# Kernel tuning notes

Hardware: AMD Instinct MI355X
Metric: run time of the kernel (lower is better)

Reference implementation:

```python
import jax, jax.numpy as jnp
import numpy as np

B = 16
S_IN, S_DIM, Z_DIM, PE_DIM = 21, 256, 64, 64
REGIONS = ["cdr3", "pep", "mhc", "hv", "hj", "lv", "lj"]
LENS = {"cdr3": 24, "pep": 16, "mhc": 48, "hv": 104, "hj": 16, "lv": 104, "lj": 14}
L_TOTAL = 1 + sum(LENS.values())  # 327 = collapse token + all regions (full masks)
N_COND = 6


def _pos_enc(L):
    # sinusoidal PE matching one_d_positional_encoding: sin for even i, cos for odd i,
    # both with divisor 10000**(i/dim)
    pos = jnp.arange(L, dtype=jnp.float32)
    i = jnp.arange(PE_DIM)
    ang = pos[:, None] / (10000.0 ** (i.astype(jnp.float32) / PE_DIM))
    return jnp.where(i % 2 == 0, jnp.sin(ang), jnp.cos(ang))  # [L, 64]


def _pair_id():
    # region label per position: 0=psi, 1=cdr3, 2..7 = conditioning regions in order
    reg = np.concatenate([[0]] + [[k + 1] * LENS[r] for k, r in enumerate(REGIONS)])
    reg = jnp.asarray(reg, dtype=jnp.int32)
    ri, rj = reg[:, None], reg[None, :]
    i = jnp.arange(L_TOTAL, dtype=jnp.int32)[:, None]
    j = jnp.arange(L_TOTAL, dtype=jnp.int32)[None, :]
    p = jnp.zeros((L_TOTAL, L_TOTAL), dtype=jnp.int32)
    p = jnp.where((i == 0) | (j == 0), 1, p)                    # lvl1: psi <-> all
    p = jnp.where((i == 0) & (j == 0), 0, p)                    # lvl0: psi self
    cb = (ri == 1) & (rj == 1)
    p = jnp.where(cb & (jnp.abs(i - j) == 1), 2, p)             # lvl2: cdr3 sequential
    p = jnp.where(cb & (i != j) & (jnp.abs(i - j) != 1), 3, p)  # lvl3: cdr3 internal
    p = jnp.where(((ri == 1) & (rj >= 2)) | ((ri >= 2) & (rj == 1)), 4, p)  # lvl4
    p = jnp.where((ri >= 2) & (ri == rj), 5 + (ri - 2), p)      # lvl5..10: cond internal
    a = jnp.minimum(ri, rj) - 2
    b = jnp.maximum(ri, rj) - 2
    cross = a * (2 * N_COND - a - 1) // 2 + (b - a - 1)         # upper-tri pair index
    p = jnp.where((ri >= 2) & (rj >= 2) & (ri != rj), 11 + cross, p)  # lvl11..25
    return jnp.minimum(p, 31)


def _region_emb(seq, w2, seq_W, seq_b, pos_W, pos_b):
    # seq: [B, Lr, 21] -> [B, Lr, 256]
    se = jnp.einsum('bld,ed->ble', seq, seq_W) + seq_b
    pe = _pos_enc(seq.shape[1]) @ pos_W.T + pos_b  # [Lr, 256]
    return w2[0] * se + w2[1] * pe


def setup_inputs() -> dict:
    key = jax.random.key(0)
    ks = jax.random.split(key, 16)
    inp = {}
    for n, (name, r) in enumerate(zip(
            ['cdr3_xt', 'pep_seq', 'mhc_seq', 'hv_seq', 'hj_seq', 'lv_seq', 'lj_seq'], REGIONS)):
        inp[name] = jax.random.normal(ks[n], (B, LENS[r], S_IN), dtype=jnp.float32)
    inp['seq_W'] = jax.random.normal(ks[7], (S_DIM, S_IN), dtype=jnp.float32) * 0.1
    inp['seq_b'] = jnp.zeros((S_DIM,), dtype=jnp.float32)
    inp['pos_W'] = jax.random.normal(ks[8], (S_DIM, PE_DIM), dtype=jnp.float32) * 0.1
    inp['pos_b'] = jnp.zeros((S_DIM,), dtype=jnp.float32)
    inp['pair1_W'] = jax.random.normal(ks[9], (Z_DIM // 2, 8), dtype=jnp.float32) * 0.3
    inp['pair1_b'] = jnp.zeros((Z_DIM // 2,), dtype=jnp.float32)
    inp['pair2_W'] = jax.random.normal(ks[10], (Z_DIM // 2, 4), dtype=jnp.float32) * 0.3
    inp['pair2_b'] = jnp.zeros((Z_DIM // 2,), dtype=jnp.float32)
    inp['collapse_token'] = jax.random.normal(ks[11], (1, S_DIM), dtype=jnp.float32) * 0.1
    inp['collapse_weight'] = jnp.ones((1,), dtype=jnp.float32)
    inp['region_w'] = jax.random.uniform(ks[12], (7, 2), dtype=jnp.float32) + 0.5
    for name, r in zip(['cdr3_mask', 'pep_mask', 'mhc_mask', 'hv_mask', 'hj_mask', 'lv_mask', 'lj_mask'], REGIONS):
        inp[name] = jnp.ones((B, LENS[r]), dtype=jnp.int32)
    return inp


def reference(cdr3_xt, pep_seq, mhc_seq, hv_seq, hj_seq, lv_seq, lj_seq,
              seq_W, seq_b, pos_W, pos_b, pair1_W, pair1_b, pair2_W, pair2_b,
              collapse_token, collapse_weight, region_w,
              cdr3_mask, pep_mask, mhc_mask, hv_mask, hj_mask, lv_mask, lj_mask):
    # masks are all-ones -> every region is full-length (static shapes); they are
    # only used in torch to derive lengths, so they are closed-over constants here.
    seqs = [cdr3_xt, pep_seq, mhc_seq, hv_seq, hj_seq, lv_seq, lj_seq]
    parts = [jnp.broadcast_to(collapse_weight * collapse_token, (B, 1, S_DIM))]
    for k, seq in enumerate(seqs):
        parts.append(_region_emb(seq, region_w[k], seq_W, seq_b, pos_W, pos_b))
    s = jnp.concatenate(parts, axis=1)  # [B, 327, 256]
    p = _pair_id()                      # [327, 327] int32, identical across batch
    # one_hot(k, n) @ W.T + b  ==  (W.T + b)[k]  -> pure gather from tiny tables
    t1 = pair1_W.T + pair1_b            # [8, 32]
    t2 = pair2_W.T + pair2_b            # [4, 32]
    z = jnp.concatenate([t1[p // 4], t2[p % 4]], axis=-1)        # [327, 327, 64]
    z = jnp.broadcast_to(z[None], (B, L_TOTAL, L_TOTAL, Z_DIM))  # per-sample z list -> stacked
    return s, z
```

## Files before the change

kernel.cpp:

```cpp
#include <hip/hip_runtime.h>
#include <math.h>

#define NB 16
#define LTOT 327
#define SDIM 256
#define ZD 64

__device__ __constant__ int d_starts[7] = {1, 25, 41, 89, 193, 209, 313};
__device__ __constant__ int d_lens[7]   = {24, 16, 48, 104, 16, 104, 14};

__device__ __forceinline__ int regid(int x) {
    return (x >= 1) + (x >= 25) + (x >= 41) + (x >= 89) + (x >= 193) + (x >= 209) + (x >= 313);
}

__device__ __forceinline__ int pair_id(int i, int j, int ri, int rj) {
    if ((i == 0) && (j == 0)) return 0;
    if ((i == 0) || (j == 0)) return 1;
    if ((ri == 1) && (rj == 1)) {
        int d = i > j ? i - j : j - i;
        if (d == 1) return 2;
        if (d != 0) return 3;
        return 0;
    }
    if ((ri == 1) || (rj == 1)) return 4;
    if (ri == rj) return 5 + ri - 2;
    int a = (ri < rj ? ri : rj) - 2;
    int c = (ri < rj ? rj : ri) - 2;
    return 11 + a * (11 - a) / 2 + (c - a - 1);
}

__global__ __launch_bounds__(256) void s_kernel(
    const float* __restrict__ s0, const float* __restrict__ s1,
    const float* __restrict__ s2, const float* __restrict__ s3,
    const float* __restrict__ s4, const float* __restrict__ s5,
    const float* __restrict__ s6,
    const float* __restrict__ seqW, const float* __restrict__ seqb,
    const float* __restrict__ posW, const float* __restrict__ posb,
    const float* __restrict__ ctok, const float* __restrict__ cw,
    const float* __restrict__ rw,
    float* __restrict__ out)
{
    int blk = blockIdx.x;
    int l = blk % LTOT;
    int b = blk / LTOT;
    int e = threadIdx.x;

    if (l == 0) {
        out[(size_t)blk * SDIM + e] = cw[0] * ctok[e];
        return;
    }

    __shared__ float sh_seq[21];
    __shared__ float sh_pe[64];

    int k = (l >= 25) + (l >= 41) + (l >= 89) + (l >= 193) + (l >= 209) + (l >= 313);
    int pl = l - d_starts[k];

    const float* sp;
    switch (k) {
        case 0: sp = s0; break; case 1: sp = s1; break; case 2: sp = s2; break;
        case 3: sp = s3; break; case 4: sp = s4; break; case 5: sp = s5; break;
        default: sp = s6;
    }
    if (e < 21) sh_seq[e] = sp[((size_t)b * d_lens[k] + pl) * 21 + e];
    if (e < 64) {
        float scale = exp2f(-(float)e * (13.287712379549449f / 64.0f));
        float ang = (float)pl * scale;
        sh_pe[e] = (e & 1) ? cosf(ang) : sinf(ang);
    }
    __syncthreads();

    float se = seqb[e];
    const float* wrow = seqW + e * 21;
    #pragma unroll
    for (int d = 0; d < 21; d++) se = fmaf(sh_seq[d], wrow[d], se);

    float pe = posb[e];
    const float* pwrow = posW + e * 64;
    #pragma unroll 8
    for (int i2 = 0; i2 < 64; i2++) pe = fmaf(sh_pe[i2], pwrow[i2], pe);

    float w0 = rw[2 * k], w1 = rw[2 * k + 1];
    out[(size_t)blk * SDIM + e] = w0 * se + w1 * pe;
}

#define TSTRIDE 68

__global__ __launch_bounds__(256) void z_kernel(
    const float* __restrict__ p1W, const float* __restrict__ p1b,
    const float* __restrict__ p2W, const float* __restrict__ p2b,
    float* __restrict__ outz)
{
    __shared__ __align__(16) float table[32 * TSTRIDE];
    __shared__ int pr[LTOT];

    int t = threadIdx.x;

    for (int idx = t; idx < 32 * 64; idx += 256) {
        int p = idx >> 6, c = idx & 63;
        float v;
        if (c < 32) v = p1W[c * 8 + (p >> 2)] + p1b[c];
        else        v = p2W[(c - 32) * 4 + (p & 3)] + p2b[c - 32];
        table[p * TSTRIDE + c] = v;
    }

    int blk = blockIdx.x;
    int i = blk % LTOT;
    int ri = regid(i);
    for (int j = t; j < LTOT; j += 256) pr[j] = pair_id(i, j, ri, regid(j));
    __syncthreads();

    float4* dst = (float4*)(outz + (size_t)blk * (LTOT * ZD));
    const int NF4 = LTOT * (ZD / 4);
    for (int idx = t; idx < NF4; idx += 256) {
        int j = idx >> 4, c4 = idx & 15;
        const float4* src = (const float4*)(table + pr[j] * TSTRIDE + c4 * 4);
        dst[idx] = *src;
    }
}

extern "C" void kernel_launch(void* const* d_in, const int* in_sizes, int n_in,
                              void* d_out, int out_size, void* d_ws, size_t ws_size,
                              hipStream_t stream) {
    const float* seq0 = (const float*)d_in[0];
    const float* seq1 = (const float*)d_in[1];
    const float* seq2 = (const float*)d_in[2];
    const float* seq3 = (const float*)d_in[3];
    const float* seq4 = (const float*)d_in[4];
    const float* seq5 = (const float*)d_in[5];
    const float* seq6 = (const float*)d_in[6];
    const float* seqW = (const float*)d_in[7];
    const float* seqb = (const float*)d_in[8];
    const float* posW = (const float*)d_in[9];
    const float* posb = (const float*)d_in[10];
    const float* p1W  = (const float*)d_in[11];
    const float* p1b  = (const float*)d_in[12];
    const float* p2W  = (const float*)d_in[13];
    const float* p2b  = (const float*)d_in[14];
    const float* ctok = (const float*)d_in[15];
    const float* cw   = (const float*)d_in[16];
    const float* rw   = (const float*)d_in[17];

    float* out = (float*)d_out;
    float* outz = out + (size_t)NB * LTOT * SDIM;

    s_kernel<<<NB * LTOT, 256, 0, stream>>>(seq0, seq1, seq2, seq3, seq4, seq5, seq6,
                                            seqW, seqb, posW, posb, ctok, cw, rw, out);
    z_kernel<<<NB * LTOT, 256, 0, stream>>>(p1W, p1b, p2W, p2b, outz);
}
```

Before: 543.1 us.

## Hoist positional encoding out of batch loop and write z by region segments

Positional-encoding projections are computed once per position into workspace by a new kernel, since they do not depend on the batch. The s kernel then only does the 21-wide sequence projection and adds the precomputed term. The z kernel drops the per-column pair-id shared array and writes each region segment with one table value, handling the cdr3-cdr3 diagonal band specially. Kernel launch order changes and one launch is added; the fallback is used only if the workspace is too small.

```diff
diff --git a/kernel.cpp b/kernel.cpp
--- a/kernel.cpp
+++ b/kernel.cpp
@@ -8,6 +8,9 @@
 
 __device__ __constant__ int d_starts[7] = {1, 25, 41, 89, 193, 209, 313};
 __device__ __constant__ int d_lens[7]   = {24, 16, 48, 104, 16, 104, 14};
+
+__device__ __constant__ int seg_s[8] = {0, 1, 25, 41, 89, 193, 209, 313};
+__device__ __constant__ int seg_e[8] = {1, 25, 41, 89, 193, 209, 313, 327};
 
 __device__ __forceinline__ int regid(int x) {
     return (x >= 1) + (x >= 25) + (x >= 41) + (x >= 89) + (x >= 193) + (x >= 209) + (x >= 313);
@@ -27,6 +30,69 @@
     int a = (ri < rj ? ri : rj) - 2;
     int c = (ri < rj ? rj : ri) - 2;
     return 11 + a * (11 - a) / 2 + (c - a - 1);
+}
+
+__global__ __launch_bounds__(256) void pe_kernel(
+    const float* __restrict__ posW, const float* __restrict__ posb,
+    const float* __restrict__ rw, float* __restrict__ pe_full)
+{
+    int l = blockIdx.x;
+    int e = threadIdx.x;
+    __shared__ float sh_pe[64];
+
+    int k = (l >= 25) + (l >= 41) + (l >= 89) + (l >= 193) + (l >= 209) + (l >= 313);
+    int pl = (l == 0) ? 0 : (l - d_starts[k]);
+    if (e < 64) {
+        float scale = exp2f(-(float)e * (13.287712379549449f / 64.0f));
+        float ang = (float)pl * scale;
+        sh_pe[e] = (e & 1) ? cosf(ang) : sinf(ang);
+    }
+    __syncthreads();
+
+    float pe = posb[e];
+    const float* pwrow = posW + e * 64;
+    #pragma unroll 8
+    for (int i2 = 0; i2 < 64; i2++) pe = fmaf(sh_pe[i2], pwrow[i2], pe);
+    pe_full[(size_t)l * SDIM + e] = rw[2 * k + 1] * pe;
+}
+
+__global__ __launch_bounds__(256) void s_kernel2(
+    const float* __restrict__ s0, const float* __restrict__ s1,
+    const float* __restrict__ s2, const float* __restrict__ s3,
+    const float* __restrict__ s4, const float* __restrict__ s5,
+    const float* __restrict__ s6,
+    const float* __restrict__ seqW, const float* __restrict__ seqb,
+    const float* __restrict__ ctok, const float* __restrict__ cw,
+    const float* __restrict__ rw, const float* __restrict__ pe_full,
+    float* __restrict__ out)
+{
+    int blk = blockIdx.x;
+    int l = blk % LTOT;
+    int b = blk / LTOT;
+    int e = threadIdx.x;
+
+    if (l == 0) {
+        out[(size_t)blk * SDIM + e] = cw[0] * ctok[e];
+        return;
+    }
+    __shared__ float sh_seq[21];
+    int k = (l >= 25) + (l >= 41) + (l >= 89) + (l >= 193) + (l >= 209) + (l >= 313);
+    int pl = l - d_starts[k];
+    const float* sp;
+    switch (k) {
+        case 0: sp = s0; break; case 1: sp = s1; break; case 2: sp = s2; break;
+        case 3: sp = s3; break; case 4: sp = s4; break; case 5: sp = s5; break;
+        default: sp = s6;
+    }
+    if (e < 21) sh_seq[e] = sp[((size_t)b * d_lens[k] + pl) * 21 + e];
+    __syncthreads();
+
+    float se = seqb[e];
+    const float* wrow = seqW + e * 21;
+    #pragma unroll
+    for (int d = 0; d < 21; d++) se = fmaf(sh_seq[d], wrow[d], se);
+
+    out[(size_t)blk * SDIM + e] = rw[2 * k] * se + pe_full[(size_t)l * SDIM + e];
 }
 
 __global__ __launch_bounds__(256) void s_kernel(
@@ -44,18 +110,11 @@
     int l = blk % LTOT;
     int b = blk / LTOT;
     int e = threadIdx.x;
-
-    if (l == 0) {
-        out[(size_t)blk * SDIM + e] = cw[0] * ctok[e];
-        return;
-    }
-
+    if (l == 0) { out[(size_t)blk * SDIM + e] = cw[0] * ctok[e]; return; }
     __shared__ float sh_seq[21];
     __shared__ float sh_pe[64];
-
     int k = (l >= 25) + (l >= 41) + (l >= 89) + (l >= 193) + (l >= 209) + (l >= 313);
     int pl = l - d_starts[k];
-
     const float* sp;
     switch (k) {
         case 0: sp = s0; break; case 1: sp = s1; break; case 2: sp = s2; break;
@@ -69,19 +128,15 @@
         sh_pe[e] = (e & 1) ? cosf(ang) : sinf(ang);
     }
     __syncthreads();
-
     float se = seqb[e];
     const float* wrow = seqW + e * 21;
     #pragma unroll
     for (int d = 0; d < 21; d++) se = fmaf(sh_seq[d], wrow[d], se);
-
     float pe = posb[e];
     const float* pwrow = posW + e * 64;
     #pragma unroll 8
     for (int i2 = 0; i2 < 64; i2++) pe = fmaf(sh_pe[i2], pwrow[i2], pe);
-
-    float w0 = rw[2 * k], w1 = rw[2 * k + 1];
-    out[(size_t)blk * SDIM + e] = w0 * se + w1 * pe;
+    out[(size_t)blk * SDIM + e] = rw[2 * k] * se + rw[2 * k + 1] * pe;
 }
 
 #define TSTRIDE 68
@@ -92,8 +147,6 @@
     float* __restrict__ outz)
 {
     __shared__ __align__(16) float table[32 * TSTRIDE];
-    __shared__ int pr[LTOT];
-
     int t = threadIdx.x;
 
     for (int idx = t; idx < 32 * 64; idx += 256) {
@@ -103,19 +156,35 @@
         else        v = p2W[(c - 32) * 4 + (p & 3)] + p2b[c - 32];
         table[p * TSTRIDE + c] = v;
     }
+    __syncthreads();
 
     int blk = blockIdx.x;
     int i = blk % LTOT;
     int ri = regid(i);
-    for (int j = t; j < LTOT; j += 256) pr[j] = pair_id(i, j, ri, regid(j));
-    __syncthreads();
+    int c4 = t & 15;
+    int jo = t >> 4;
 
     float4* dst = (float4*)(outz + (size_t)blk * (LTOT * ZD));
-    const int NF4 = LTOT * (ZD / 4);
-    for (int idx = t; idx < NF4; idx += 256) {
-        int j = idx >> 4, c4 = idx & 15;
-        const float4* src = (const float4*)(table + pr[j] * TSTRIDE + c4 * 4);
-        dst[idx] = *src;
+
+    #pragma unroll
+    for (int s = 0; s < 8; s++) {
+        int js = seg_s[s], je = seg_e[s];
+        if (ri == 1 && s == 1) {
+            float4 v0 = *(const float4*)(table + 0 * TSTRIDE + c4 * 4);
+            float4 v2 = *(const float4*)(table + 2 * TSTRIDE + c4 * 4);
+            float4 v3 = *(const float4*)(table + 3 * TSTRIDE + c4 * 4);
+            for (int j = js + jo; j < je; j += 16) {
+                int d = i > j ? i - j : j - i;
+                float4 v = (d == 0) ? v0 : ((d == 1) ? v2 : v3);
+                dst[j * 16 + c4] = v;
+            }
+        } else {
+            int p = pair_id(i, js, ri, regid(js));
+            float4 v = *(const float4*)(table + p * TSTRIDE + c4 * 4);
+            for (int j = js + jo; j < je; j += 16) {
+                dst[j * 16 + c4] = v;
+            }
+        }
     }
 }
 
@@ -144,7 +213,15 @@
     float* out = (float*)d_out;
     float* outz = out + (size_t)NB * LTOT * SDIM;
 
-    s_kernel<<<NB * LTOT, 256, 0, stream>>>(seq0, seq1, seq2, seq3, seq4, seq5, seq6,
-                                            seqW, seqb, posW, posb, ctok, cw, rw, out);
     z_kernel<<<NB * LTOT, 256, 0, stream>>>(p1W, p1b, p2W, p2b, outz);
-}
+
+    if (ws_size >= (size_t)LTOT * SDIM * sizeof(float)) {
+        float* pe_full = (float*)d_ws;
+        pe_kernel<<<LTOT, 256, 0, stream>>>(posW, posb, rw, pe_full);
+        s_kernel2<<<NB * LTOT, 256, 0, stream>>>(seq0, seq1, seq2, seq3, seq4, seq5, seq6,
+                                                 seqW, seqb, ctok, cw, rw, pe_full, out);
+    } else {
+        s_kernel<<<NB * LTOT, 256, 0, stream>>>(seq0, seq1, seq2, seq3, seq4, seq5, seq6,
+                                                seqW, seqb, posW, posb, ctok, cw, rw, out);
+    }
+}
```

Measured after the change: 509.8 us (median of 2 runs). 6.1% less time.

## Fuse s and z kernels, specialize z writes per region with nontemporal stores

Applied to the files above, without the earlier changes.

Merges the s-embedding and z-pair kernels into one launch, with the z blocks placed first and the s blocks after them. The z path no longer builds a per-row pair-id array in shared memory. It loops over the 8 static region segments, loads one table vector per segment (the cdr3-cdr3 block picks per element), and writes it with nontemporal stores. This removes a launch and most of the per-element shared-memory gathers on a write-bound output of about 27M floats, at the cost of a more complex control flow.

```diff
diff --git a/kernel.cpp b/kernel.cpp
--- a/kernel.cpp
+++ b/kernel.cpp
@@ -5,9 +5,9 @@
 #define LTOT 327
 #define SDIM 256
 #define ZD 64
+#define ZROWS (NB * LTOT)
 
-__device__ __constant__ int d_starts[7] = {1, 25, 41, 89, 193, 209, 313};
-__device__ __constant__ int d_lens[7]   = {24, 16, 48, 104, 16, 104, 14};
+typedef float vf4 __attribute__((ext_vector_type(4)));
 
 __device__ __forceinline__ int regid(int x) {
     return (x >= 1) + (x >= 25) + (x >= 41) + (x >= 89) + (x >= 193) + (x >= 209) + (x >= 313);
@@ -29,93 +29,104 @@
     return 11 + a * (11 - a) / 2 + (c - a - 1);
 }
 
-__global__ __launch_bounds__(256) void s_kernel(
+__global__ __launch_bounds__(256) void fused_kernel(
     const float* __restrict__ s0, const float* __restrict__ s1,
     const float* __restrict__ s2, const float* __restrict__ s3,
     const float* __restrict__ s4, const float* __restrict__ s5,
     const float* __restrict__ s6,
     const float* __restrict__ seqW, const float* __restrict__ seqb,
     const float* __restrict__ posW, const float* __restrict__ posb,
+    const float* __restrict__ p1W, const float* __restrict__ p1b,
+    const float* __restrict__ p2W, const float* __restrict__ p2b,
     const float* __restrict__ ctok, const float* __restrict__ cw,
     const float* __restrict__ rw,
-    float* __restrict__ out)
+    float* __restrict__ out, float* __restrict__ outz)
 {
+    __shared__ __align__(16) float shbuf[32 * 68];
     int blk = blockIdx.x;
-    int l = blk % LTOT;
-    int b = blk / LTOT;
-    int e = threadIdx.x;
-
-    if (l == 0) {
-        out[(size_t)blk * SDIM + e] = cw[0] * ctok[e];
-        return;
-    }
-
-    __shared__ float sh_seq[21];
-    __shared__ float sh_pe[64];
-
-    int k = (l >= 25) + (l >= 41) + (l >= 89) + (l >= 193) + (l >= 209) + (l >= 313);
-    int pl = l - d_starts[k];
-
-    const float* sp;
-    switch (k) {
-        case 0: sp = s0; break; case 1: sp = s1; break; case 2: sp = s2; break;
-        case 3: sp = s3; break; case 4: sp = s4; break; case 5: sp = s5; break;
-        default: sp = s6;
-    }
-    if (e < 21) sh_seq[e] = sp[((size_t)b * d_lens[k] + pl) * 21 + e];
-    if (e < 64) {
-        float scale = exp2f(-(float)e * (13.287712379549449f / 64.0f));
-        float ang = (float)pl * scale;
-        sh_pe[e] = (e & 1) ? cosf(ang) : sinf(ang);
-    }
-    __syncthreads();
-
-    float se = seqb[e];
-    const float* wrow = seqW + e * 21;
-    #pragma unroll
-    for (int d = 0; d < 21; d++) se = fmaf(sh_seq[d], wrow[d], se);
-
-    float pe = posb[e];
-    const float* pwrow = posW + e * 64;
-    #pragma unroll 8
-    for (int i2 = 0; i2 < 64; i2++) pe = fmaf(sh_pe[i2], pwrow[i2], pe);
-
-    float w0 = rw[2 * k], w1 = rw[2 * k + 1];
-    out[(size_t)blk * SDIM + e] = w0 * se + w1 * pe;
-}
-
-#define TSTRIDE 68
-
-__global__ __launch_bounds__(256) void z_kernel(
-    const float* __restrict__ p1W, const float* __restrict__ p1b,
-    const float* __restrict__ p2W, const float* __restrict__ p2b,
-    float* __restrict__ outz)
-{
-    __shared__ __align__(16) float table[32 * TSTRIDE];
-    __shared__ int pr[LTOT];
-
     int t = threadIdx.x;
 
-    for (int idx = t; idx < 32 * 64; idx += 256) {
-        int p = idx >> 6, c = idx & 63;
-        float v;
-        if (c < 32) v = p1W[c * 8 + (p >> 2)] + p1b[c];
-        else        v = p2W[(c - 32) * 4 + (p & 3)] + p2b[c - 32];
-        table[p * TSTRIDE + c] = v;
-    }
+    if (blk < ZROWS) {
+        for (int idx = t; idx < 32 * 64; idx += 256) {
+            int p = idx >> 6, c = idx & 63;
+            float v = (c < 32) ? p1W[c * 8 + (p >> 2)] + p1b[c]
+                               : p2W[(c - 32) * 4 + (p & 3)] + p2b[c - 32];
+            shbuf[p * 68 + c] = v;
+        }
+        __syncthreads();
 
-    int blk = blockIdx.x;
-    int i = blk % LTOT;
-    int ri = regid(i);
-    for (int j = t; j < LTOT; j += 256) pr[j] = pair_id(i, j, ri, regid(j));
-    __syncthreads();
+        int i = blk % LTOT;
+        int ri = regid(i);
+        int c4 = t & 15;
+        int jo = t >> 4;
+        vf4* dst = (vf4*)(outz + (size_t)blk * (LTOT * ZD));
 
-    float4* dst = (float4*)(outz + (size_t)blk * (LTOT * ZD));
-    const int NF4 = LTOT * (ZD / 4);
-    for (int idx = t; idx < NF4; idx += 256) {
-        int j = idx >> 4, c4 = idx & 15;
-        const float4* src = (const float4*)(table + pr[j] * TSTRIDE + c4 * 4);
-        dst[idx] = *src;
+        constexpr int ss_[8] = {0, 1, 25, 41, 89, 193, 209, 313};
+        constexpr int se_[8] = {1, 25, 41, 89, 193, 209, 313, 327};
+
+        #pragma unroll
+        for (int s = 0; s < 8; s++) {
+            const int js = ss_[s], je = se_[s];
+            if (s == 1 && ri == 1) {
+                vf4 v0 = *(const vf4*)(shbuf + 0 * 68 + c4 * 4);
+                vf4 v2 = *(const vf4*)(shbuf + 2 * 68 + c4 * 4);
+                vf4 v3 = *(const vf4*)(shbuf + 3 * 68 + c4 * 4);
+                #pragma unroll
+                for (int j = js + jo; j < je; j += 16) {
+                    int d = i > j ? i - j : j - i;
+                    vf4 v = (d == 0) ? v0 : ((d == 1) ? v2 : v3);
+                    __builtin_nontemporal_store(v, dst + j * 16 + c4);
+                }
+            } else {
+                int p = pair_id(i, js, ri, s);
+                vf4 v = *(const vf4*)(shbuf + p * 68 + c4 * 4);
+                #pragma unroll
+                for (int j = js + jo; j < je; j += 16) {
+                    __builtin_nontemporal_store(v, dst + j * 16 + c4);
+                }
+            }
+        }
+    } else {
+        blk -= ZROWS;
+        int l = blk % LTOT;
+        int b = blk / LTOT;
+        int e = t;
+
+        if (l == 0) {
+            out[(size_t)blk * SDIM + e] = cw[0] * ctok[e];
+            return;
+        }
+        constexpr int starts_[7] = {1, 25, 41, 89, 193, 209, 313};
+        constexpr int lens_[7]   = {24, 16, 48, 104, 16, 104, 14};
+        int k = (l >= 25) + (l >= 41) + (l >= 89) + (l >= 193) + (l >= 209) + (l >= 313);
+        int pl = l - starts_[k];
+        const float* sp;
+        switch (k) {
+            case 0: sp = s0; break; case 1: sp = s1; break; case 2: sp = s2; break;
+            case 3: sp = s3; break; case 4: sp = s4; break; case 5: sp = s5; break;
+            default: sp = s6;
+        }
+        float* sh_seq = shbuf;
+        float* sh_pe  = shbuf + 32;
+        if (e < 21) sh_seq[e] = sp[((size_t)b * lens_[k] + pl) * 21 + e];
+        if (e < 64) {
+            float scale = exp2f(-(float)e * (13.287712379549449f / 64.0f));
+            float ang = (float)pl * scale;
+            sh_pe[e] = (e & 1) ? cosf(ang) : sinf(ang);
+        }
+        __syncthreads();
+
+        float se = seqb[e];
+        const float* wrow = seqW + e * 21;
+        #pragma unroll
+        for (int d = 0; d < 21; d++) se = fmaf(sh_seq[d], wrow[d], se);
+
+        float pe = posb[e];
+        const float* pwrow = posW + e * 64;
+        #pragma unroll 8
+        for (int i2 = 0; i2 < 64; i2++) pe = fmaf(sh_pe[i2], pwrow[i2], pe);
+
+        out[(size_t)blk * SDIM + e] = rw[2 * k] * se + rw[2 * k + 1] * pe;
     }
 }
 
@@ -144,7 +155,8 @@
     float* out = (float*)d_out;
     float* outz = out + (size_t)NB * LTOT * SDIM;
 
-    s_kernel<<<NB * LTOT, 256, 0, stream>>>(seq0, seq1, seq2, seq3, seq4, seq5, seq6,
-                                            seqW, seqb, posW, posb, ctok, cw, rw, out);
-    z_kernel<<<NB * LTOT, 256, 0, stream>>>(p1W, p1b, p2W, p2b, outz);
+    fused_kernel<<<2 * ZROWS, 256, 0, stream>>>(seq0, seq1, seq2, seq3, seq4, seq5, seq6,
+                                                seqW, seqb, posW, posb,
+                                                p1W, p1b, p2W, p2b,
+                                                ctok, cw, rw, out, outz);
 }
```

After: 521.5 us. 1.04x faster.
